# Optimization experiments

Measured on AMD Instinct MI355X. Metric: run time of the kernel, lower is better.

## Reference

```python
import jax, jax.numpy as jnp
import numpy as np

D_MODEL = 1536
NUM_HEADS = 16
QUERY_GROUPS = 4
HEAD_DIM = D_MODEL // NUM_HEADS  # 96
HEADS_PER_GROUP = NUM_HEADS // QUERY_GROUPS
THETA = 10000.0


def _grid_positions(grid_t, grid_h, grid_w):
    # [N, 3] lookup table of (t, h, w) coords, N = T*H*W, 'ij' meshgrid order
    t, h, w = jnp.meshgrid(jnp.arange(grid_t), jnp.arange(grid_h), jnp.arange(grid_w), indexing='ij')
    return jnp.stack([t.reshape(-1), h.reshape(-1), w.reshape(-1)], axis=-1)


def _rope3d(x, positions):
    # x: [B, N, H, head_dim]; rotate three contiguous head_dim//3 slices, one per axis
    B, N, H, hd = x.shape
    dpa = hd // 3            # dims per axis
    P = dpa // 2             # rotation pairs per axis
    freqs = 1.0 / (THETA ** (jnp.arange(P, dtype=jnp.float32) * 2.0 / dpa))  # same for t/h/w
    parts = []
    for axis in range(3):
        ang = positions[:, axis].astype(jnp.float32)[:, None] * freqs[None, :]  # [N, P]
        cos = jnp.cos(ang)[None, :, None, :]  # [1, N, 1, P]
        sin = jnp.sin(ang)[None, :, None, :]
        sl = x[..., axis * dpa:(axis + 1) * dpa].reshape(B, N, H, P, 2)
        x0, x1 = sl[..., 0], sl[..., 1]
        rot = jnp.stack([x0 * cos - x1 * sin, x0 * sin + x1 * cos], axis=-1)
        parts.append(rot.reshape(B, N, H, dpa))
    return jnp.concatenate(parts, axis=-1)


def setup_inputs() -> dict:
    key = jax.random.key(0)
    k1, k2, k3 = jax.random.split(key, 3)
    B, GT, GH, GW = 2, 8, 16, 16
    N = GT * GH * GW  # 2048
    x = jax.random.normal(k1, (B, N, D_MODEL), dtype=jnp.float32)
    qkv_out = NUM_HEADS * HEAD_DIM + 2 * QUERY_GROUPS * HEAD_DIM  # 2304
    w_qkv = jax.random.normal(k2, (qkv_out, D_MODEL), dtype=jnp.float32) * 0.02
    w_o = jax.random.normal(k3, (D_MODEL, D_MODEL), dtype=jnp.float32) * 0.02
    return {"x": x, "w_qkv": w_qkv, "w_o": w_o, "grid_t": GT, "grid_h": GH, "grid_w": GW}


def reference(x, w_qkv, w_o, grid_t, grid_h, grid_w):
    B, N, _ = x.shape
    qkv = x @ w_qkv.T  # [B, N, 2304]
    q_dim = NUM_HEADS * HEAD_DIM
    kv_dim = QUERY_GROUPS * HEAD_DIM
    q = qkv[..., :q_dim].reshape(B, N, NUM_HEADS, HEAD_DIM)
    k = qkv[..., q_dim:q_dim + kv_dim].reshape(B, N, QUERY_GROUPS, HEAD_DIM)
    v = qkv[..., q_dim + kv_dim:].reshape(B, N, QUERY_GROUPS, HEAD_DIM)

    pos = _grid_positions(grid_t, grid_h, grid_w)  # [N, 3]
    q = _rope3d(q, pos)
    k = _rope3d(k, pos)

    # GQA: repeat_interleave kv heads up to num_heads
    k = jnp.repeat(k, HEADS_PER_GROUP, axis=2)
    v = jnp.repeat(v, HEADS_PER_GROUP, axis=2)

    scale = 1.0 / jnp.sqrt(jnp.asarray(HEAD_DIM, dtype=x.dtype))
    scores = jnp.einsum('bnhd,bmhd->bhnm', q, k) * scale
    attn = jax.nn.softmax(scores, axis=-1)
    out = jnp.einsum('bhnm,bmhd->bnhd', attn, v).reshape(B, N, D_MODEL)
    return out @ w_o.T
```

## Files before the change

kernel.cpp:

```cpp
#include <hip/hip_runtime.h>
#include <hip/hip_bf16.h>

typedef short bf16x8 __attribute__((ext_vector_type(8)));
typedef float f32x4  __attribute__((ext_vector_type(4)));

#define NH    16
#define NG    4
#define HD    96
#define DM    1536
#define BB    2
#define NSEQ  2048
#define QKVD  2304
#define MROWS (BB * NSEQ)

__device__ __forceinline__ short bf16_bits(float v)
{
    __hip_bfloat16 h = __float2bfloat16(v);
    return *reinterpret_cast<short*>(&h);
}

__device__ __forceinline__ float bf16_val(short v)
{
    __hip_bfloat16 h = *reinterpret_cast<__hip_bfloat16*>(&v);
    return __bfloat162float(h);
}

__device__ __forceinline__ void stage16(short* dst, const float* src)
{
    float f[16];
    *(float4*)(f + 0)  = *(const float4*)(src + 0);
    *(float4*)(f + 4)  = *(const float4*)(src + 4);
    *(float4*)(f + 8)  = *(const float4*)(src + 8);
    *(float4*)(f + 12) = *(const float4*)(src + 12);
    bf16x8 v0, v1;
    #pragma unroll
    for (int j = 0; j < 8; ++j) { v0[j] = bf16_bits(f[j]); v1[j] = bf16_bits(f[8 + j]); }
    *(bf16x8*)dst = v0;
    *(bf16x8*)(dst + 8) = v1;
}
__device__ __forceinline__ void stage16(short* dst, const __hip_bfloat16* src)
{
    *(bf16x8*)dst       = *(const bf16x8*)src;
    *(bf16x8*)(dst + 8) = *(const bf16x8*)(src + 8);
}

__device__ __forceinline__ void store_c(__hip_bfloat16* p, float v)
{
    *p = __float2bfloat16(v);
}
__device__ __forceinline__ void store_c(float* p, float v) { *p = v; }

__device__ __forceinline__ void gload_lds16(const short* g, short* lds)
{
    __builtin_amdgcn_global_load_lds(
        (const __attribute__((address_space(1))) unsigned int*)g,
        (__attribute__((address_space(3))) unsigned int*)lds,
        16, 0, 0);
}

__global__ __launch_bounds__(256) void cvt3_bf16(
    const float* __restrict__ x,  short* __restrict__ xb,
    const float* __restrict__ wq, short* __restrict__ wqb,
    const float* __restrict__ wo, short* __restrict__ wob)
{
    const int i = blockIdx.x * 256 + threadIdx.x;
    const float* s; short* d; int off;
    if (i < 786432)       { s = x;  d = xb;  off = i; }
    else if (i < 1228800) { s = wq; d = wqb; off = i - 786432; }
    else                  { s = wo; d = wob; off = i - 1228800; }
    float f[8];
    *(float4*)(f + 0) = *(const float4*)(s + (size_t)off * 8);
    *(float4*)(f + 4) = *(const float4*)(s + (size_t)off * 8 + 4);
    bf16x8 v;
    #pragma unroll
    for (int j = 0; j < 8; ++j) v[j] = bf16_bits(f[j]);
    *(bf16x8*)(d + (size_t)off * 8) = v;
}

template <typename TC>
__global__ __launch_bounds__(256) void gemm_async(
    const short* __restrict__ A,
    const short* __restrict__ B,
    TC* __restrict__ C,
    int M, int Nc, int K, int lda, int ldb, int nbx)
{
    __shared__ __align__(16) short As[128][32];
    __shared__ __align__(16) short Bs[128][32];

    const int tid  = threadIdx.x;
    const int wave = tid >> 6;
    const int lane = tid & 63;
    const int quad = lane >> 4;
    const int l16  = lane & 15;
    const int wm = (wave >> 1) * 64;
    const int wn = (wave & 1) * 64;

    const int cpx = gridDim.x >> 3;
    const int swz = (blockIdx.x & 7) * cpx + (blockIdx.x >> 3);
    const int bx  = swz % nbx;
    const int by  = swz / nbx;
    const int m0 = by * 128;
    const int n0 = bx * 128;

    const int lrow = lane >> 2;
    const int lcol = (lane & 3) * 8;

    f32x4 acc[4][4] = {};

    for (int k0 = 0; k0 < K; k0 += 32) {
        __syncthreads();
        #pragma unroll
        for (int i = 0; i < 2; ++i) {
            const int j = wave * 2 + i;
            gload_lds16(A + (size_t)(m0 + j * 16 + lrow) * lda + k0 + lcol, &As[j * 16][0]);
            gload_lds16(B + (size_t)(n0 + j * 16 + lrow) * ldb + k0 + lcol, &Bs[j * 16][0]);
        }
        __syncthreads();

        bf16x8 af[4], bfr[4];
        #pragma unroll
        for (int i = 0; i < 4; ++i)
            af[i] = *(const bf16x8*)&As[wm + i * 16 + l16][quad * 8];
        #pragma unroll
        for (int j = 0; j < 4; ++j)
            bfr[j] = *(const bf16x8*)&Bs[wn + j * 16 + l16][quad * 8];
        #pragma unroll
        for (int i = 0; i < 4; ++i)
            #pragma unroll
            for (int j = 0; j < 4; ++j)
                acc[i][j] = __builtin_amdgcn_mfma_f32_16x16x32_bf16(
                    af[i], bfr[j], acc[i][j], 0, 0, 0);
    }

    #pragma unroll
    for (int i = 0; i < 4; ++i)
      #pragma unroll
      for (int j = 0; j < 4; ++j)
        #pragma unroll
        for (int r = 0; r < 4; ++r) {
            const int row = m0 + wm + i * 16 + quad * 4 + r;
            const int col = n0 + wn + j * 16 + l16;
            store_c(C + (size_t)row * Nc + col, acc[i][j][r]);
        }
}

#define KSTR 40

template <typename TA, typename TB, typename TC>
__global__ __launch_bounds__(256) void gemm_tiled(
    const TA* __restrict__ A,
    const TB* __restrict__ B,
    TC* __restrict__ C,
    int M, int Nc, int K, int lda)
{
    __shared__ __align__(16) short As[128][KSTR];
    __shared__ __align__(16) short Bs[128][KSTR];

    const int tid  = threadIdx.x;
    const int wave = tid >> 6;
    const int lane = tid & 63;
    const int quad = lane >> 4;
    const int l16  = lane & 15;
    const int wm = (wave >> 1) * 64;
    const int wn = (wave & 1) * 64;
    const int m0 = blockIdx.y * 128;
    const int n0 = blockIdx.x * 128;

    const int srow  = tid >> 1;
    const int skseg = (tid & 1) << 4;
    const TA* Asrc = A + (size_t)(m0 + srow) * lda + skseg;
    const TB* Bsrc = B + (size_t)(n0 + srow) * K + skseg;

    f32x4 acc[4][4] = {};

    for (int k0 = 0; k0 < K; k0 += 32) {
        __syncthreads();
        stage16(&As[srow][skseg], Asrc + k0);
        stage16(&Bs[srow][skseg], Bsrc + k0);
        __syncthreads();

        bf16x8 af[4], bfr[4];
        #pragma unroll
        for (int i = 0; i < 4; ++i)
            af[i] = *(const bf16x8*)&As[wm + i * 16 + l16][quad * 8];
        #pragma unroll
        for (int j = 0; j < 4; ++j)
            bfr[j] = *(const bf16x8*)&Bs[wn + j * 16 + l16][quad * 8];
        #pragma unroll
        for (int i = 0; i < 4; ++i)
            #pragma unroll
            for (int j = 0; j < 4; ++j)
                acc[i][j] = __builtin_amdgcn_mfma_f32_16x16x32_bf16(
                    af[i], bfr[j], acc[i][j], 0, 0, 0);
    }

    #pragma unroll
    for (int i = 0; i < 4; ++i)
      #pragma unroll
      for (int j = 0; j < 4; ++j)
        #pragma unroll
        for (int r = 0; r < 4; ++r) {
            const int row = m0 + wm + i * 16 + quad * 4 + r;
            const int col = n0 + wn + j * 16 + l16;
            store_c(C + (size_t)row * Nc + col, acc[i][j][r]);
        }
}

#define KVSTRIDE 196608

__global__ __launch_bounds__(256) void kv_prep(
    const __hip_bfloat16* __restrict__ qkv,
    short* __restrict__ Kbuf,
    short* __restrict__ Vtbuf)
{
    const int e    = blockIdx.x * 256 + threadIdx.x;
    const int p2   = e % 48;
    const int t2   = e / 48;
    const int slot = t2 & 7;
    const int r    = t2 >> 3;
    const int n    = r & (NSEQ - 1);
    const int b    = r >> 11;

    const int axis = p2 >> 4;
    const int lp   = p2 & 15;
    const int d0   = axis * 32 + 2 * lp;

    if (slot >= 4) {
        const int g  = slot - 4;
        const int bg = b * NG + g;
        const short* p = (const short*)(qkv + (size_t)r * QKVD + DM + NG * HD + g * HD + d0);
        const short v0 = p[0];
        const short v1 = p[1];
        short* vb = Vtbuf + (size_t)bg * KVSTRIDE;
        const int tbase = (n >> 6) * 12 + ((n & 63) >> 5);
        const int qoff  = ((n >> 3) & 3) << 4;
        const int eidx  = n & 7;
        vb[((size_t)(tbase + (d0 >> 4) * 2) << 9) + (qoff + (d0 & 15)) * 8 + eidx] = v0;
        vb[((size_t)(tbase + ((d0 + 1) >> 4) * 2) << 9) + (qoff + ((d0 + 1) & 15)) * 8 + eidx] = v1;
        return;
    }

    const int pt = n >> 8;
    const int ph = (n >> 4) & 15;
    const int pw = n & 15;
    const int pos  = (axis == 0) ? pt : ((axis == 1) ? ph : pw);
    const float freq = exp2f(-(float)lp * 0.8304820237f);
    float s, c;
    sincosf((float)pos * freq, &s, &c);

    const int g  = slot;
    const int bg = b * NG + g;
    const __hip_bfloat16* p = qkv + (size_t)r * QKVD + DM + g * HD + d0;
    const float x0 = __bfloat162float(p[0]);
    const float x1 = __bfloat162float(p[1]);
    short* kb = Kbuf + (size_t)bg * KVSTRIDE
              + ((size_t)((n >> 4) * 3 + (d0 >> 5)) << 9)
              + ((((d0 >> 3) & 3) << 4) + (n & 15)) * 8 + (d0 & 7);
    kb[0] = bf16_bits(x0 * c - x1 * s);
    kb[1] = bf16_bits(x0 * s + x1 * c);
}

#define QT 128
#define KC 64
#define PSTR 72

__global__ __launch_bounds__(512) void flash_attn(
    __hip_bfloat16* __restrict__ qkv,
    const short* __restrict__ Kbuf,
    const short* __restrict__ Vtbuf)
{
    __shared__ __align__(16) short KsLin[6144];
    __shared__ __align__(16) short VtLin[6144];
    __shared__ __align__(16) short Pw[8][16][PSTR];

    const int tid  = threadIdx.x;
    const int wave = tid >> 6;
    const int lane = tid & 63;
    const int quad = lane >> 4;
    const int l16  = lane & 15;

    const int id  = blockIdx.x;
    const int bg  = id & 7;
    const int k   = id >> 3;
    const int b   = bg >> 2, g = bg & 3;
    const int h   = g * 4 + (k & 3);
    const int n0  = (k >> 2) * QT;

    const short* Kc = Kbuf  + (size_t)bg * KVSTRIDE;
    const short* Vc = Vtbuf + (size_t)bg * KVSTRIDE;
    const int lane8 = lane * 8;

    const int nrow = n0 + wave * 16 + l16;
    const __hip_bfloat16* Qb = qkv + (size_t)(b * NSEQ + nrow) * QKVD + h * HD;
    const float posv[3] = { (float)(nrow >> 8), (float)((nrow >> 4) & 15), (float)(nrow & 15) };
    bf16x8 qa[3];
    #pragma unroll
    for (int kk = 0; kk < 3; ++kk) {
        bf16x8 q = *(const bf16x8*)(Qb + kk * 32 + quad * 8);
        #pragma unroll
        for (int i = 0; i < 4; ++i) {
            const int lp = quad * 4 + i;
            const float freq = exp2f(-(float)lp * 0.8304820237f);
            float s, c;
            sincosf(posv[kk] * freq, &s, &c);
            const float x0 = bf16_val(q[2 * i]);
            const float x1 = bf16_val(q[2 * i + 1]);
            q[2 * i]     = bf16_bits(x0 * c - x1 * s);
            q[2 * i + 1] = bf16_bits(x0 * s + x1 * c);
        }
        qa[kk] = q;
    }

    f32x4 o[6] = {};
    float psum[4] = {0.f, 0.f, 0.f, 0.f};
    const float c1 = 0.14724434f;
    const float c2 = -5.7707802f;
    const int sw = l16 >> 2;

    for (int j0 = 0; j0 < NSEQ; j0 += KC) {
        __syncthreads();
        {
            const short* Kch = Kc + ((size_t)((j0 >> 4) * 3) << 9);
            const short* Vch = Vc + ((size_t)((j0 >> 6) * 12) << 9);
            const short* sb = (wave < 4) ? Kch : Vch;
            short* db       = (wave < 4) ? KsLin : VtLin;
            #pragma unroll
            for (int i = 0; i < 3; ++i) {
                const int t = (wave & 3) * 3 + i;
                gload_lds16(sb + ((size_t)t << 9) + lane8, db + (t << 9));
            }
        }
        __syncthreads();

        f32x4 S[4] = {};
        #pragma unroll
        for (int nt = 0; nt < 4; ++nt) {
            bf16x8 kf[3];
            #pragma unroll
            for (int kk = 0; kk < 3; ++kk)
                kf[kk] = *(const bf16x8*)&KsLin[((nt * 3 + kk) << 9) + lane8];
            #pragma unroll
            for (int kk = 0; kk < 3; ++kk)
                S[nt] = __builtin_amdgcn_mfma_f32_16x16x32_bf16(qa[kk], kf[kk], S[nt], 0, 0, 0);
        }

        #pragma unroll
        for (int nt = 0; nt < 4; ++nt) {
            const int cb   = nt * 2 + (l16 >> 3);
            const int colp = ((cb ^ quad) << 3) + (l16 & 7);
            #pragma unroll
            for (int r = 0; r < 4; ++r) {
                const float p = exp2f(fmaf(S[nt][r], c1, c2));
                psum[r] += p;
                Pw[wave][quad * 4 + r][colp] = bf16_bits(p);
            }
        }

        bf16x8 pa0 = *(const bf16x8*)&Pw[wave][l16][(quad ^ sw) << 3];
        bf16x8 pa1 = *(const bf16x8*)&Pw[wave][l16][((quad ^ sw) + 4) << 3];
        #pragma unroll
        for (int dt = 0; dt < 6; ++dt) {
            bf16x8 vb0 = *(const bf16x8*)&VtLin[((dt * 2 + 0) << 9) + lane8];
            bf16x8 vb1 = *(const bf16x8*)&VtLin[((dt * 2 + 1) << 9) + lane8];
            o[dt] = __builtin_amdgcn_mfma_f32_16x16x32_bf16(pa0, vb0, o[dt], 0, 0, 0);
            o[dt] = __builtin_amdgcn_mfma_f32_16x16x32_bf16(pa1, vb1, o[dt], 0, 0, 0);
        }
    }

    #pragma unroll
    for (int off = 1; off < 16; off <<= 1)
        #pragma unroll
        for (int r = 0; r < 4; ++r)
            psum[r] += __shfl_xor(psum[r], off);
    float inv_l[4];
    #pragma unroll
    for (int r = 0; r < 4; ++r) inv_l[r] = 1.f / psum[r];

    #pragma unroll
    for (int dt = 0; dt < 6; ++dt)
        #pragma unroll
        for (int r = 0; r < 4; ++r) {
            __hip_bfloat16* op =
                qkv + (size_t)(b * NSEQ + n0 + wave * 16 + quad * 4 + r) * QKVD
                    + h * HD + dt * 16 + l16;
            *op = __float2bfloat16(o[dt][r] * inv_l[r]);
        }
}

extern "C" void kernel_launch(void* const* d_in, const int* in_sizes, int n_in,
                              void* d_out, int out_size, void* d_ws, size_t ws_size,
                              hipStream_t stream)
{
    const float* x    = (const float*)d_in[0];
    const float* wqkv = (const float*)d_in[1];
    const float* wo   = (const float*)d_in[2];

    __hip_bfloat16* qkv = (__hip_bfloat16*)d_ws;
    short* xb    = (short*)d_out;
    short* wqb   = (short*)((char*)d_out + 12582912);
    short* Kbuf  = (short*)d_out;
    short* Vtbuf = (short*)((char*)d_out + 3145728);

    const bool wo_in_ws = ws_size >= 23592960;
    short* wob = wo_in_ws ? (short*)((char*)d_ws + 18874368) : (short*)d_out;

    cvt3_bf16<<<wo_in_ws ? 5952 : 4800, 256, 0, stream>>>(x, xb, wqkv, wqb, wo, wob);

    gemm_async<__hip_bfloat16>
        <<<(QKVD / 128) * (MROWS / 128), 256, 0, stream>>>(
            xb, wqb, qkv, MROWS, QKVD, DM, DM, DM, QKVD / 128);

    kv_prep<<<(MROWS * 8 * 48) / 256, 256, 0, stream>>>(qkv, Kbuf, Vtbuf);

    flash_attn<<<dim3(NSEQ / QT * BB * NH, 1), 512, 0, stream>>>(qkv, Kbuf, Vtbuf);

    if (wo_in_ws) {
        gemm_async<float>
            <<<(DM / 128) * (MROWS / 128), 256, 0, stream>>>(
                (const short*)qkv, wob, (float*)d_out, MROWS, DM, DM, QKVD, DM, DM / 128);
    } else {
        gemm_tiled<__hip_bfloat16, float, float>
            <<<dim3(DM / 128, MROWS / 128), 256, 0, stream>>>(
                qkv, wo, (float*)d_out, MROWS, DM, DM, QKVD);
    }
}
```

Baseline: 274.7 us.

## Fuse K RoPE and K/V relayout into QKV GEMM epilogue

Adds a QKV GEMM variant whose epilogue writes Q normally, applies 3D RoPE to K columns via lane shuffles, and scatters K and transposed V straight into the tiled buffers flash attention expects. This removes the separate kv_prep kernel and its round trip through global memory. K/V buffers move into workspace when it is large enough. The epilogue now does scattered 2-byte stores and per-element sincos, which may cost more than the launch it saves.

```diff
diff --git a/kernel.cpp b/kernel.cpp
--- a/kernel.cpp
+++ b/kernel.cpp
@@ -77,6 +77,128 @@
     *(bf16x8*)(d + (size_t)off * 8) = v;
 }
 
+#define KVSTRIDE 196608
+
+__global__ __launch_bounds__(256) void gemm_qkv_fused(
+    const short* __restrict__ A,
+    const short* __restrict__ B,
+    __hip_bfloat16* __restrict__ C,
+    short* __restrict__ Kbuf,
+    short* __restrict__ Vtbuf)
+{
+    __shared__ __align__(16) short As[128][32];
+    __shared__ __align__(16) short Bs[128][32];
+
+    const int tid  = threadIdx.x;
+    const int wave = tid >> 6;
+    const int lane = tid & 63;
+    const int quad = lane >> 4;
+    const int l16  = lane & 15;
+    const int wm = (wave >> 1) * 64;
+    const int wn = (wave & 1) * 64;
+
+    const int cpx = gridDim.x >> 3;
+    const int swz = (blockIdx.x & 7) * cpx + (blockIdx.x >> 3);
+    const int bx  = swz % 18;
+    const int by  = swz / 18;
+    const int m0 = by * 128;
+    const int n0 = bx * 128;
+
+    const int lrow = lane >> 2;
+    const int lcol = (lane & 3) * 8;
+
+    f32x4 acc[4][4] = {};
+
+    for (int k0 = 0; k0 < DM; k0 += 32) {
+        __syncthreads();
+        #pragma unroll
+        for (int i = 0; i < 2; ++i) {
+            const int j = wave * 2 + i;
+            gload_lds16(A + (size_t)(m0 + j * 16 + lrow) * DM + k0 + lcol, &As[j * 16][0]);
+            gload_lds16(B + (size_t)(n0 + j * 16 + lrow) * DM + k0 + lcol, &Bs[j * 16][0]);
+        }
+        __syncthreads();
+
+        bf16x8 af[4], bfr[4];
+        #pragma unroll
+        for (int i = 0; i < 4; ++i)
+            af[i] = *(const bf16x8*)&As[wm + i * 16 + l16][quad * 8];
+        #pragma unroll
+        for (int j = 0; j < 4; ++j)
+            bfr[j] = *(const bf16x8*)&Bs[wn + j * 16 + l16][quad * 8];
+        #pragma unroll
+        for (int i = 0; i < 4; ++i)
+            #pragma unroll
+            for (int j = 0; j < 4; ++j)
+                acc[i][j] = __builtin_amdgcn_mfma_f32_16x16x32_bf16(
+                    af[i], bfr[j], acc[i][j], 0, 0, 0);
+    }
+
+    if (n0 < 1536) {
+        #pragma unroll
+        for (int i = 0; i < 4; ++i)
+          #pragma unroll
+          for (int j = 0; j < 4; ++j)
+            #pragma unroll
+            for (int r = 0; r < 4; ++r) {
+                const int row = m0 + wm + i * 16 + quad * 4 + r;
+                const int col = n0 + wn + j * 16 + l16;
+                store_c(C + (size_t)row * QKVD + col, acc[i][j][r]);
+            }
+    } else if (n0 < 1920) {
+        #pragma unroll
+        for (int j = 0; j < 4; ++j) {
+            const int col = n0 + wn + j * 16 + l16;
+            const int cg  = col - 1536;
+            const int g   = cg / 96;
+            const int d   = cg - g * 96;
+            const int axis = d >> 5;
+            const int lp   = (d & 31) >> 1;
+            const float freq = exp2f(-(float)lp * 0.8304820237f);
+            #pragma unroll
+            for (int i = 0; i < 4; ++i)
+                #pragma unroll
+                for (int r = 0; r < 4; ++r) {
+                    const int row = m0 + wm + i * 16 + quad * 4 + r;
+                    const int n  = row & (NSEQ - 1);
+                    const int bb = row >> 11;
+                    const float v  = acc[i][j][r];
+                    const float pv = __shfl_xor(v, 1);
+                    const int pos = (axis == 0) ? (n >> 8)
+                                  : (axis == 1) ? ((n >> 4) & 15) : (n & 15);
+                    float sn, cs;
+                    sincosf((float)pos * freq, &sn, &cs);
+                    const float out = ((d & 1) == 0) ? (v * cs - pv * sn)
+                                                     : (pv * sn + v * cs);
+                    short* kb = Kbuf + (size_t)(bb * NG + g) * KVSTRIDE
+                              + ((size_t)((n >> 4) * 3 + (d >> 5)) << 9)
+                              + ((((d >> 3) & 3) << 4) + (n & 15)) * 8 + (d & 7);
+                    *kb = bf16_bits(out);
+                }
+        }
+    } else {
+        #pragma unroll
+        for (int j = 0; j < 4; ++j) {
+            const int col = n0 + wn + j * 16 + l16;
+            const int cg  = col - 1920;
+            const int g   = cg / 96;
+            const int d   = cg - g * 96;
+            #pragma unroll
+            for (int i = 0; i < 4; ++i)
+                #pragma unroll
+                for (int r = 0; r < 4; ++r) {
+                    const int row = m0 + wm + i * 16 + quad * 4 + r;
+                    const int n  = row & (NSEQ - 1);
+                    const int bb = row >> 11;
+                    short* vb = Vtbuf + (size_t)(bb * NG + g) * KVSTRIDE
+                              + ((size_t)((n >> 6) * 12 + ((n & 63) >> 5) + (d >> 4) * 2) << 9)
+                              + ((((n >> 3) & 3) << 4) + (d & 15)) * 8 + (n & 7);
+                    *vb = bf16_bits(acc[i][j][r]);
+                }
+        }
+    }
+}
+
 template <typename TC>
 __global__ __launch_bounds__(256) void gemm_async(
     const short* __restrict__ A,
@@ -205,8 +327,6 @@
             store_c(C + (size_t)row * Nc + col, acc[i][j][r]);
         }
 }
-
-#define KVSTRIDE 196608
 
 __global__ __launch_bounds__(256) void kv_prep(
     const __hip_bfloat16* __restrict__ qkv,
@@ -398,19 +518,26 @@
     __hip_bfloat16* qkv = (__hip_bfloat16*)d_ws;
     short* xb    = (short*)d_out;
     short* wqb   = (short*)((char*)d_out + 12582912);
-    short* Kbuf  = (short*)d_out;
-    short* Vtbuf = (short*)((char*)d_out + 3145728);
 
     const bool wo_in_ws = ws_size >= 23592960;
+    const bool fuse_kv  = ws_size >= 29884416;
     short* wob = wo_in_ws ? (short*)((char*)d_ws + 18874368) : (short*)d_out;
 
+    short* Kbuf  = fuse_kv ? (short*)((char*)d_ws + 23592960) : (short*)d_out;
+    short* Vtbuf = fuse_kv ? (short*)((char*)d_ws + 26738688)
+                           : (short*)((char*)d_out + 3145728);
+
     cvt3_bf16<<<wo_in_ws ? 5952 : 4800, 256, 0, stream>>>(x, xb, wqkv, wqb, wo, wob);
 
-    gemm_async<__hip_bfloat16>
-        <<<(QKVD / 128) * (MROWS / 128), 256, 0, stream>>>(
-            xb, wqb, qkv, MROWS, QKVD, DM, DM, DM, QKVD / 128);
-
-    kv_prep<<<(MROWS * 8 * 48) / 256, 256, 0, stream>>>(qkv, Kbuf, Vtbuf);
+    if (fuse_kv) {
+        gemm_qkv_fused<<<(QKVD / 128) * (MROWS / 128), 256, 0, stream>>>(
+            xb, wqb, qkv, Kbuf, Vtbuf);
+    } else {
+        gemm_async<__hip_bfloat16>
+            <<<(QKVD / 128) * (MROWS / 128), 256, 0, stream>>>(
+                xb, wqb, qkv, MROWS, QKVD, DM, DM, DM, QKVD / 128);
+        kv_prep<<<(MROWS * 8 * 48) / 256, 256, 0, stream>>>(qkv, Kbuf, Vtbuf);
+    }
 
     flash_attn<<<dim3(NSEQ / QT * BB * NH, 1), 512, 0, stream>>>(qkv, Kbuf, Vtbuf);
 
```

After: 785.3 us. +185.8%, slower.
